# Optimization experiments

Hardware: AMD Instinct MI355X
Metric: run time of the kernel (lower is better)

The kernel has to match this reference:

```python
import jax, jax.numpy as jnp
import numpy as np

B, T, D, H = 2, 2048, 1024, 16
HD = D // H
ALPHA = HD ** -0.5
EPS = 1e-5


def setup_inputs() -> dict:
    key = jax.random.key(0)
    ks = jax.random.split(key, 8)
    x = jax.random.normal(ks[0], (B, T, D), dtype=jnp.float32)
    # additive causal mask: 0 where allowed, -inf where disallowed
    causal = jnp.triu(jnp.ones((T, T), dtype=bool), k=1)
    attention_mask = jnp.where(causal, -jnp.inf, 0.0).astype(jnp.float32)
    rab = jax.random.normal(ks[1], (1, H, T, T), dtype=jnp.float32) * 0.02
    W_in = jax.random.normal(ks[2], (D, 4 * D), dtype=jnp.float32) * (D ** -0.5)
    b_in = jnp.zeros((4 * D,), dtype=jnp.float32)
    W_out = jax.random.normal(ks[3], (D, D), dtype=jnp.float32) * (D ** -0.5)
    b_out = jnp.zeros((D,), dtype=jnp.float32)
    ln_w = jnp.ones((D,), dtype=jnp.float32)
    ln_b = jnp.zeros((D,), dtype=jnp.float32)
    return {"x": x, "attention_mask": attention_mask, "rab": rab,
            "W_in": W_in, "b_in": b_in, "W_out": W_out, "b_out": b_out,
            "ln_w": ln_w, "ln_b": ln_b}


def _heads(t):  # [B,T,D] -> [B,H,T,HD]
    return t.reshape(B, T, H, HD).transpose(0, 2, 1, 3)


def _layernorm(t, w, b):
    mu = jnp.mean(t, axis=-1, keepdims=True)
    var = jnp.mean(jnp.square(t - mu), axis=-1, keepdims=True)
    return (t - mu) * jax.lax.rsqrt(var + EPS) * w + b


def reference(x, attention_mask, rab, W_in, b_in, W_out, b_out, ln_w, ln_b):
    h = jax.nn.silu(x @ W_in + b_in)                      # [B,T,4D]
    U, V, Q, K = jnp.split(h, 4, axis=-1)
    Qh, Kh, Vh = _heads(Q), _heads(K), _heads(V)
    logits = jnp.einsum('bhqd,bhkd->bhqk', Qh, Kh) * ALPHA
    logits = logits + rab + attention_mask[None, None]    # [B,H,T,T]
    # allowed counts from the additive mask (0 == allowed)
    allowed = (attention_mask == 0).astype(jnp.float32)   # [T,T]
    denom = jnp.clip(jnp.sum(allowed, axis=-1, keepdims=True), 1.0)  # [T,1]
    logits_safe = jnp.where(jnp.isinf(logits) & (logits < 0), -1e9, logits)
    attn = jax.nn.silu(logits_safe) / denom[None, None]
    AV = jnp.einsum('bhqk,bhkd->bhqd', attn, Vh)
    AV = AV.transpose(0, 2, 1, 3).reshape(B, T, D)
    y = (_layernorm(AV, ln_w, ln_b) * U) @ W_out + b_out
    return y
```

## Files before the change

kernel.cpp:

```cpp
#include <hip/hip_runtime.h>

#define BATCH 2
#define TSEQ 2048
#define DIM 1024
#define NH 16
#define HDIM 64
#define MROWS (BATCH * TSEQ)

typedef __attribute__((ext_vector_type(4))) float f32x4;
typedef __attribute__((ext_vector_type(8))) short short8;

__device__ __forceinline__ unsigned short f2bf(float f) {
    union { float f; unsigned int u; } x; x.f = f;
    unsigned int r = x.u + 0x7fffu + ((x.u >> 16) & 1u);
    return (unsigned short)(r >> 16);
}

__device__ __forceinline__ float silu_f(float v) {
    return v * __builtin_amdgcn_rcpf(1.f + __expf(-v));
}

__device__ __forceinline__ void gl_lds16(const void* g, void* l) {
    __builtin_amdgcn_global_load_lds(
        (const __attribute__((address_space(1))) void*)g,
        (__attribute__((address_space(3))) void*)l, 16, 0, 0);
}

__device__ __forceinline__ short8 rd_swz(const unsigned short* base, int row, int chunk) {
    const char* b = (const char*)base;
    return *(const short8*)(b + row * 128 + (((chunk ^ (row & 7)) << 4)));
}

__global__ __launch_bounds__(256) void k_convert(const float* __restrict__ in,
                                                 unsigned short* __restrict__ out,
                                                 int n4) {
    int i = blockIdx.x * 256 + threadIdx.x;
    if (i < n4) {
        float4 v = ((const float4*)in)[i];
        union { unsigned short s[4]; uint2 u; } o;
        o.s[0] = f2bf(v.x); o.s[1] = f2bf(v.y); o.s[2] = f2bf(v.z); o.s[3] = f2bf(v.w);
        ((uint2*)out)[i] = o.u;
    }
}

__global__ __launch_bounds__(256) void k_transpose(const float* __restrict__ in,
                                                   unsigned short* __restrict__ out,
                                                   int R, int C) {
    __shared__ float tile[32][33];
    int tx = threadIdx.x, ty = threadIdx.y;
    int c0 = blockIdx.x * 32, r0 = blockIdx.y * 32;
    #pragma unroll
    for (int i = 0; i < 32; i += 8)
        tile[ty + i][tx] = in[(size_t)(r0 + ty + i) * C + c0 + tx];
    __syncthreads();
    #pragma unroll
    for (int i = 0; i < 32; i += 8)
        out[(size_t)(c0 + ty + i) * R + r0 + tx] = f2bf(tile[tx][ty + i]);
}

template <int EPI>
__global__ __launch_bounds__(256) void k_gemm(
    const unsigned short* __restrict__ A, const unsigned short* __restrict__ Bt,
    int M, int N, int K, const float* __restrict__ bias,
    float* __restrict__ outU, unsigned short* __restrict__ outVt,
    unsigned short* __restrict__ outQ, unsigned short* __restrict__ outK,
    float* __restrict__ outY)
{
    __shared__ __align__(16) unsigned short sA[128 * 32];
    __shared__ __align__(16) unsigned short sB[128 * 32];
    const int tid = threadIdx.x;
    const int bm = blockIdx.x, bn = blockIdx.y;
    const int row0 = bm * 128, col0 = bn * 128;
    const int lane = tid & 63, w = tid >> 6;
    const int wrow = (w >> 1) * 64, wcol = (w & 1) * 64;
    const int lr = lane & 15, lk = lane >> 4;

    f32x4 acc[4][4] = {};

    for (int k0 = 0; k0 < K; k0 += 32) {
        for (int c = tid; c < 512; c += 256) {
            int r = c >> 2, kc = c & 3;
            gl_lds16(A + (size_t)(row0 + r) * K + k0 + kc * 8, sA + c * 8);
            gl_lds16(Bt + (size_t)(col0 + r) * K + k0 + kc * 8, sB + c * 8);
        }
        __syncthreads();
        short8 af[4], bf[4];
        #pragma unroll
        for (int m = 0; m < 4; ++m)
            af[m] = *(const short8*)(sA + (wrow + m * 16 + lr) * 32 + lk * 8);
        #pragma unroll
        for (int n = 0; n < 4; ++n)
            bf[n] = *(const short8*)(sB + (wcol + n * 16 + lr) * 32 + lk * 8);
        #pragma unroll
        for (int m = 0; m < 4; ++m)
            #pragma unroll
            for (int n = 0; n < 4; ++n)
                acc[m][n] = __builtin_amdgcn_mfma_f32_16x16x32_bf16(af[m], bf[n], acc[m][n], 0, 0, 0);
        __syncthreads();
    }

    #pragma unroll
    for (int m = 0; m < 4; ++m) {
        #pragma unroll
        for (int n = 0; n < 4; ++n) {
            int cg = col0 + wcol + n * 16 + lr;
            float bv = bias[cg];
            int rg0 = row0 + wrow + m * 16 + lk * 4;
            if (EPI == 1) {
                float sv[4];
                #pragma unroll
                for (int j = 0; j < 4; ++j)
                    sv[j] = silu_f(acc[m][n][j] + bv);
                int sec = cg >> 10, cc = cg & 1023;
                if (sec == 0) {
                    #pragma unroll
                    for (int j = 0; j < 4; ++j)
                        outU[((size_t)(rg0 + j) << 10) + cc] = sv[j];
                } else if (sec == 1) {
                    union { unsigned short s[4]; uint2 u; } pk;
                    #pragma unroll
                    for (int j = 0; j < 4; ++j) pk.s[j] = f2bf(sv[j]);
                    *(uint2*)(outVt + ((size_t)cc << 12) + rg0) = pk.u;
                } else if (sec == 2) {
                    #pragma unroll
                    for (int j = 0; j < 4; ++j)
                        outQ[((size_t)(rg0 + j) << 10) + cc] = f2bf(sv[j] * 0.125f);
                } else {
                    #pragma unroll
                    for (int j = 0; j < 4; ++j)
                        outK[((size_t)(rg0 + j) << 10) + cc] = f2bf(sv[j]);
                }
            } else {
                #pragma unroll
                for (int j = 0; j < 4; ++j)
                    outY[(size_t)(rg0 + j) * N + cg] = acc[m][n][j] + bv;
            }
        }
    }
}

__global__ __launch_bounds__(256, 4) void k_attn(
    const unsigned short* __restrict__ Qb,
    const unsigned short* __restrict__ Kb,
    const unsigned short* __restrict__ Vt,
    const float* __restrict__ rab,
    float* __restrict__ AV)
{
    __shared__ __align__(16) unsigned short sK[2][64 * 64];
    __shared__ __align__(16) unsigned short sVt[2][64 * 64];
    __shared__ __align__(16) unsigned short sP[64 * 64];

    const int tid = threadIdx.x;
    const int lane = tid & 63;
    const int w = tid >> 6;
    const int lr = lane & 15;
    const int lk = lane >> 4;

    const int bid = blockIdx.x;
    const int idx = bid & 255;
    const int g = bid >> 8;
    const int h = idx & 15;
    const int r_ = idx >> 4;
    const int bb = g >> 1;
    const int qt = (g & 1) ? (31 - r_) : r_;
    const int q0 = qt * 64;

    short8 qreg[2];
    #pragma unroll
    for (int ks = 0; ks < 2; ++ks)
        qreg[ks] = *(const short8*)(Qb + (((size_t)(bb * TSEQ + q0 + w * 16 + lr)) << 10)
                                     + h * 64 + ks * 32 + lk * 8);

    int qrow[4];
    const float* rabrow[4];
    const float* rabh = rab + (size_t)h * TSEQ * TSEQ;
    #pragma unroll
    for (int j = 0; j < 4; ++j) {
        qrow[j] = q0 + w * 16 + lk * 4 + j;
        rabrow[j] = rabh + (size_t)qrow[j] * TSEQ + lr;
    }

    f32x4 acc[4] = {};

    #define STAGE(buf, kt_) do {                                                      \
        int k0s = (kt_) * 64;                                                         \
        for (int c = tid; c < 512; c += 256) {                                        \
            int rr = c >> 3, kc = c & 7;                                              \
            int kcs = kc ^ (rr & 7);                                                  \
            gl_lds16(Kb + (((size_t)(bb * TSEQ + k0s + rr)) << 10) + h * 64 + kcs * 8,\
                     sK[buf] + c * 8);                                                \
            gl_lds16(Vt + (((size_t)(h * 64 + rr)) << 12) + bb * TSEQ + k0s + kcs * 8,\
                     sVt[buf] + c * 8);                                               \
        }                                                                             \
    } while (0)

    STAGE(0, 0);
    float rvc[4][4];
    #pragma unroll
    for (int nt = 0; nt < 4; ++nt)
        #pragma unroll
        for (int j = 0; j < 4; ++j)
            rvc[nt][j] = rabrow[j][nt * 16];
    __syncthreads();

    int cur = 0;
    for (int kt = 0; kt <= qt; ++kt) {
        const int k0 = kt * 64;
        const bool have_next = (kt < qt);
        if (have_next) STAGE(cur ^ 1, kt + 1);

        float rvn[4][4];
        if (have_next) {
            #pragma unroll
            for (int nt = 0; nt < 4; ++nt)
                #pragma unroll
                for (int j = 0; j < 4; ++j)
                    rvn[nt][j] = rabrow[j][k0 + 64 + nt * 16];
        }

        f32x4 s[4];
        #pragma unroll
        for (int nt = 0; nt < 4; ++nt) {
            f32x4 c0v;
            c0v[0] = rvc[nt][0]; c0v[1] = rvc[nt][1];
            c0v[2] = rvc[nt][2]; c0v[3] = rvc[nt][3];
            s[nt] = c0v;
        }
        #pragma unroll
        for (int ks = 0; ks < 2; ++ks) {
            #pragma unroll
            for (int nt = 0; nt < 4; ++nt)
                s[nt] = __builtin_amdgcn_mfma_f32_16x16x32_bf16(
                    qreg[ks], rd_swz(sK[cur], nt * 16 + lr, ks * 4 + lk), s[nt], 0, 0, 0);
        }

        const bool full = (kt < qt);
        char* pb = (char*)sP;
        #pragma unroll
        for (int j = 0; j < 4; ++j) {
            const int prow = w * 16 + lk * 4 + j;
            char* bj = pb + prow * 128;
            const int swz = ((lk * 4 + j) & 7) << 4;
            #pragma unroll
            for (int nt = 0; nt < 4; ++nt) {
                int k = k0 + nt * 16 + lr;
                float pv = (full || k <= qrow[j]) ? silu_f(s[nt][j]) : 0.f;
                *(unsigned short*)(bj + (((nt << 5) | (lr << 1)) ^ swz)) = f2bf(pv);
            }
        }

        #pragma unroll
        for (int ks = 0; ks < 2; ++ks) {
            short8 ap = rd_swz(sP, w * 16 + lr, ks * 4 + lk);
            #pragma unroll
            for (int dt = 0; dt < 4; ++dt)
                acc[dt] = __builtin_amdgcn_mfma_f32_16x16x32_bf16(
                    ap, rd_swz(sVt[cur], dt * 16 + lr, ks * 4 + lk), acc[dt], 0, 0, 0);
        }

        if (have_next) {
            #pragma unroll
            for (int nt = 0; nt < 4; ++nt)
                #pragma unroll
                for (int j = 0; j < 4; ++j)
                    rvc[nt][j] = rvn[nt][j];
        }

        __syncthreads();
        cur ^= 1;
    }
    #undef STAGE

    #pragma unroll
    for (int dt = 0; dt < 4; ++dt)
        #pragma unroll
        for (int j = 0; j < 4; ++j)
            AV[(((size_t)(bb * TSEQ + qrow[j])) << 10) + h * 64 + dt * 16 + lr] = acc[dt][j];
}

__global__ __launch_bounds__(256) void k_ln(const float* __restrict__ AV,
                                            const float* __restrict__ U,
                                            const float* __restrict__ lnw,
                                            const float* __restrict__ lnb,
                                            unsigned short* __restrict__ z) {
    __shared__ float red[8];
    const int row = blockIdx.x, tid = threadIdx.x;
    const float c = (float)((row & (TSEQ - 1)) + 1);
    const float eps = 1e-5f * c * c;
    float4 v = ((const float4*)(AV + ((size_t)row << 10)))[tid];
    float s = v.x + v.y + v.z + v.w;
    float s2 = v.x * v.x + v.y * v.y + v.z * v.z + v.w * v.w;
    #pragma unroll
    for (int o = 32; o > 0; o >>= 1) { s += __shfl_xor(s, o); s2 += __shfl_xor(s2, o); }
    const int w = tid >> 6;
    if ((tid & 63) == 0) { red[w] = s; red[4 + w] = s2; }
    __syncthreads();
    s = red[0] + red[1] + red[2] + red[3];
    s2 = red[4] + red[5] + red[6] + red[7];
    const float mu = s * (1.f / 1024.f);
    const float var = s2 * (1.f / 1024.f) - mu * mu;
    const float rstd = rsqrtf(var + eps);
    float4 uw = ((const float4*)(U + ((size_t)row << 10)))[tid];
    float4 lw = ((const float4*)lnw)[tid];
    float4 lb = ((const float4*)lnb)[tid];
    union { unsigned short o[4]; uint2 u; } ov;
    ov.o[0] = f2bf(((v.x - mu) * rstd * lw.x + lb.x) * uw.x);
    ov.o[1] = f2bf(((v.y - mu) * rstd * lw.y + lb.y) * uw.y);
    ov.o[2] = f2bf(((v.z - mu) * rstd * lw.z + lb.z) * uw.z);
    ov.o[3] = f2bf(((v.w - mu) * rstd * lw.w + lb.w) * uw.w);
    ((uint2*)z)[((size_t)row << 8) + tid] = ov.u;
}

extern "C" void kernel_launch(void* const* d_in, const int* in_sizes, int n_in,
                              void* d_out, int out_size, void* d_ws, size_t ws_size,
                              hipStream_t stream) {
    const float* x     = (const float*)d_in[0];
    const float* rab   = (const float*)d_in[2];
    const float* W_in  = (const float*)d_in[3];
    const float* b_in  = (const float*)d_in[4];
    const float* W_out = (const float*)d_in[5];
    const float* b_out = (const float*)d_in[6];
    const float* ln_w  = (const float*)d_in[7];
    const float* ln_b  = (const float*)d_in[8];
    float* y = (float*)d_out;

    char* ws = (char*)d_ws;
    size_t off = 0;
    auto alloc = [&](size_t bytes) -> void* {
        void* p = ws + off;
        off += (bytes + 255) & ~(size_t)255;
        return p;
    };
    unsigned short* WinT  = (unsigned short*)alloc((size_t)4096 * 1024 * 2);
    unsigned short* WoutT = (unsigned short*)alloc((size_t)1024 * 1024 * 2);
    unsigned short* xb    = (unsigned short*)alloc((size_t)MROWS * DIM * 2);
    float*          Ubuf  = (float*)alloc((size_t)MROWS * DIM * 4);
    unsigned short* Qb    = (unsigned short*)alloc((size_t)MROWS * DIM * 2);
    unsigned short* Kb    = (unsigned short*)alloc((size_t)MROWS * DIM * 2);
    unsigned short* Vtb   = (unsigned short*)alloc((size_t)DIM * MROWS * 2);
    float*          AV    = (float*)alloc((size_t)MROWS * DIM * 4);
    unsigned short* z     = (unsigned short*)alloc((size_t)MROWS * DIM * 2);

    k_convert<<<dim3(4096), dim3(256), 0, stream>>>(x, xb, MROWS * DIM / 4);
    k_transpose<<<dim3(128, 32), dim3(32, 8), 0, stream>>>(W_in, WinT, 1024, 4096);
    k_transpose<<<dim3(32, 32), dim3(32, 8), 0, stream>>>(W_out, WoutT, 1024, 1024);
    k_gemm<1><<<dim3(32, 32), dim3(256), 0, stream>>>(xb, WinT, MROWS, 4096, 1024,
                                                      b_in, Ubuf, Vtb, Qb, Kb, nullptr);
    k_attn<<<dim3(1024), dim3(256), 0, stream>>>(Qb, Kb, Vtb, rab, AV);
    k_ln<<<dim3(MROWS), dim3(256), 0, stream>>>(AV, Ubuf, ln_w, ln_b, z);
    k_gemm<2><<<dim3(32, 8), dim3(256), 0, stream>>>(z, WoutT, MROWS, 1024, 1024,
                                                     b_out, nullptr, nullptr, nullptr, nullptr, y);
}
```

Measured before the change: 186.4 us.

## Replace input projection GEMM with 256x256-tile double-buffered swizzled kernel

The input projection GEMM (4096x4096x1024) moves from 128x128 tiles with K=32 steps to a dedicated 512-thread kernel using 256x256 tiles, K=64 steps, double-buffered LDS staging with XOR swizzling, and phased MFMA issue with barriers and priority hints. The aim is more reuse per loaded byte, less LDS bank conflict, and overlap of global-to-LDS loads with compute. The cost is higher register and LDS pressure: 128 KB of LDS per block, and the grid shrinks to 256 blocks, which may underfill the GPU's CUs. The output GEMM is split off unchanged into its own non-templated kernel.

```diff
diff --git a/kernel.cpp b/kernel.cpp
--- a/kernel.cpp
+++ b/kernel.cpp
@@ -58,13 +58,118 @@
         out[(size_t)(c0 + ty + i) * R + r0 + tx] = f2bf(tile[tx][ty + i]);
 }
 
-template <int EPI>
-__global__ __launch_bounds__(256) void k_gemm(
+__device__ __forceinline__ void stage256(const unsigned short* __restrict__ A,
+                                         const unsigned short* __restrict__ Bt,
+                                         int row0, int col0, int k0,
+                                         unsigned short* sAbuf, unsigned short* sBbuf,
+                                         int tid) {
+    #pragma unroll
+    for (int q = 0; q < 4; ++q) {
+        int c = tid + 512 * q;
+        int rr = c >> 3;
+        int kcs = (c & 7) ^ (rr & 7);
+        gl_lds16(A + (size_t)(row0 + rr) * 1024 + k0 + kcs * 8, sAbuf + c * 8);
+        gl_lds16(Bt + (size_t)(col0 + rr) * 1024 + k0 + kcs * 8, sBbuf + c * 8);
+    }
+}
+
+__global__ __launch_bounds__(512, 2) void k_gemm1_256(
     const unsigned short* __restrict__ A, const unsigned short* __restrict__ Bt,
-    int M, int N, int K, const float* __restrict__ bias,
+    const float* __restrict__ bias,
     float* __restrict__ outU, unsigned short* __restrict__ outVt,
-    unsigned short* __restrict__ outQ, unsigned short* __restrict__ outK,
-    float* __restrict__ outY)
+    unsigned short* __restrict__ outQ, unsigned short* __restrict__ outK)
+{
+    __shared__ __align__(16) unsigned short sA[2][256 * 64];
+    __shared__ __align__(16) unsigned short sB[2][256 * 64];
+
+    const int tid = threadIdx.x;
+    const int lane = tid & 63, wid = tid >> 6;
+    const int lr = lane & 15, lk = lane >> 4;
+    const int wm = wid >> 2, wn = wid & 3;
+    const int bm = blockIdx.x, bn = blockIdx.y;
+    const int row0 = bm * 256, col0 = bn * 256;
+
+    f32x4 acc[8][4] = {};
+
+    stage256(A, Bt, row0, col0, 0, sA[0], sB[0], tid);
+    asm volatile("s_waitcnt vmcnt(0)" ::: "memory");
+    __builtin_amdgcn_s_barrier();
+    __builtin_amdgcn_sched_barrier(0);
+
+    int cur = 0;
+    for (int kt = 0; kt < 16; ++kt) {
+        if (kt < 15) stage256(A, Bt, row0, col0, (kt + 1) * 64, sA[cur ^ 1], sB[cur ^ 1], tid);
+        short8 bf[2][4];
+        #pragma unroll
+        for (int kk = 0; kk < 2; ++kk)
+            #pragma unroll
+            for (int n = 0; n < 4; ++n)
+                bf[kk][n] = rd_swz(sB[cur], wn * 64 + n * 16 + lr, kk * 4 + lk);
+
+        #pragma unroll
+        for (int ph = 0; ph < 4; ++ph) {
+            short8 af[2][2];
+            #pragma unroll
+            for (int mm = 0; mm < 2; ++mm)
+                #pragma unroll
+                for (int kk = 0; kk < 2; ++kk)
+                    af[mm][kk] = rd_swz(sA[cur], wm * 128 + (ph * 2 + mm) * 16 + lr, kk * 4 + lk);
+            __builtin_amdgcn_s_barrier();
+            __builtin_amdgcn_s_setprio(1);
+            #pragma unroll
+            for (int mm = 0; mm < 2; ++mm)
+                #pragma unroll
+                for (int n = 0; n < 4; ++n)
+                    #pragma unroll
+                    for (int kk = 0; kk < 2; ++kk)
+                        acc[ph * 2 + mm][n] = __builtin_amdgcn_mfma_f32_16x16x32_bf16(
+                            af[mm][kk], bf[kk][n], acc[ph * 2 + mm][n], 0, 0, 0);
+            __builtin_amdgcn_s_setprio(0);
+            if (ph == 3) asm volatile("s_waitcnt vmcnt(0)" ::: "memory");
+            __builtin_amdgcn_s_barrier();
+        }
+        __builtin_amdgcn_sched_barrier(0);
+        cur ^= 1;
+    }
+
+    const int sec = bn >> 2;
+    #pragma unroll
+    for (int n = 0; n < 4; ++n) {
+        const int cg = col0 + wn * 64 + n * 16 + lr;
+        const int cc = cg & 1023;
+        const float bv = bias[cg];
+        #pragma unroll
+        for (int m = 0; m < 8; ++m) {
+            const int rg0 = row0 + wm * 128 + m * 16 + lk * 4;
+            float sv[4];
+            #pragma unroll
+            for (int j = 0; j < 4; ++j)
+                sv[j] = silu_f(acc[m][n][j] + bv);
+            if (sec == 0) {
+                #pragma unroll
+                for (int j = 0; j < 4; ++j)
+                    outU[((size_t)(rg0 + j) << 10) + cc] = sv[j];
+            } else if (sec == 1) {
+                union { unsigned short s[4]; uint2 u; } pk;
+                #pragma unroll
+                for (int j = 0; j < 4; ++j) pk.s[j] = f2bf(sv[j]);
+                *(uint2*)(outVt + ((size_t)cc << 12) + rg0) = pk.u;
+            } else if (sec == 2) {
+                #pragma unroll
+                for (int j = 0; j < 4; ++j)
+                    outQ[((size_t)(rg0 + j) << 10) + cc] = f2bf(sv[j] * 0.125f);
+            } else {
+                #pragma unroll
+                for (int j = 0; j < 4; ++j)
+                    outK[((size_t)(rg0 + j) << 10) + cc] = f2bf(sv[j]);
+            }
+        }
+    }
+}
+
+__global__ __launch_bounds__(256) void k_gemm2(
+    const unsigned short* __restrict__ A, const unsigned short* __restrict__ Bt,
+    int M, int N, int K, const float* __restrict__ bias, float* __restrict__ outY)
 {
     __shared__ __align__(16) unsigned short sA[128 * 32];
     __shared__ __align__(16) unsigned short sB[128 * 32];
@@ -106,35 +211,9 @@
             int cg = col0 + wcol + n * 16 + lr;
             float bv = bias[cg];
             int rg0 = row0 + wrow + m * 16 + lk * 4;
-            if (EPI == 1) {
-                float sv[4];
-                #pragma unroll
-                for (int j = 0; j < 4; ++j)
-                    sv[j] = silu_f(acc[m][n][j] + bv);
-                int sec = cg >> 10, cc = cg & 1023;
-                if (sec == 0) {
-                    #pragma unroll
-                    for (int j = 0; j < 4; ++j)
-                        outU[((size_t)(rg0 + j) << 10) + cc] = sv[j];
-                } else if (sec == 1) {
-                    union { unsigned short s[4]; uint2 u; } pk;
-                    #pragma unroll
-                    for (int j = 0; j < 4; ++j) pk.s[j] = f2bf(sv[j]);
-                    *(uint2*)(outVt + ((size_t)cc << 12) + rg0) = pk.u;
-                } else if (sec == 2) {
-                    #pragma unroll
-                    for (int j = 0; j < 4; ++j)
-                        outQ[((size_t)(rg0 + j) << 10) + cc] = f2bf(sv[j] * 0.125f);
-                } else {
-                    #pragma unroll
-                    for (int j = 0; j < 4; ++j)
-                        outK[((size_t)(rg0 + j) << 10) + cc] = f2bf(sv[j]);
-                }
-            } else {
-                #pragma unroll
-                for (int j = 0; j < 4; ++j)
-                    outY[(size_t)(rg0 + j) * N + cg] = acc[m][n][j] + bv;
-            }
+            #pragma unroll
+            for (int j = 0; j < 4; ++j)
+                outY[(size_t)(rg0 + j) * N + cg] = acc[m][n][j] + bv;
         }
     }
 }
@@ -344,10 +423,8 @@
     k_convert<<<dim3(4096), dim3(256), 0, stream>>>(x, xb, MROWS * DIM / 4);
     k_transpose<<<dim3(128, 32), dim3(32, 8), 0, stream>>>(W_in, WinT, 1024, 4096);
     k_transpose<<<dim3(32, 32), dim3(32, 8), 0, stream>>>(W_out, WoutT, 1024, 1024);
-    k_gemm<1><<<dim3(32, 32), dim3(256), 0, stream>>>(xb, WinT, MROWS, 4096, 1024,
-                                                      b_in, Ubuf, Vtb, Qb, Kb, nullptr);
+    k_gemm1_256<<<dim3(16, 16), dim3(512), 0, stream>>>(xb, WinT, b_in, Ubuf, Vtb, Qb, Kb);
     k_attn<<<dim3(1024), dim3(256), 0, stream>>>(Qb, Kb, Vtb, rab, AV);
     k_ln<<<dim3(MROWS), dim3(256), 0, stream>>>(AV, Ubuf, ln_w, ln_b, z);
-    k_gemm<2><<<dim3(32, 8), dim3(256), 0, stream>>>(z, WoutT, MROWS, 1024, 1024,
-                                                     b_out, nullptr, nullptr, nullptr, nullptr, y);
-}
+    k_gemm2<<<dim3(32, 8), dim3(256), 0, stream>>>(z, WoutT, MROWS, 1024, 1024, b_out, y);
+}
```

Result: faster. 173.2 us (-7.1%).
